# Kernel optimization log

Hardware: AMD Instinct MI355X
Metric: run time of the kernel (lower is better)

## Reference

```python
import jax, jax.numpy as jnp
import numpy as np

B, L, H = 1, 2048, 2048          # batch, seq_len, hidden_size
E, N, K, R = 4096, 16, 4, 128    # intermediate, ssm_state, conv_kernel, dt_rank


def setup_inputs() -> dict:
    key = jax.random.key(0)
    ks = jax.random.split(key, 8)
    s = 0.02
    inp = {
        "hidden_states": jax.random.normal(ks[0], (B, L, H), jnp.float32),
        "in_proj_w": jax.random.normal(ks[1], (2 * E, H), jnp.float32) * s,
        "conv_w": jax.random.normal(ks[2], (E, 1, K), jnp.float32) * s,
        "conv_b": jax.random.normal(ks[3], (E,), jnp.float32) * s,
        "x_proj_w": jax.random.normal(ks[4], (R + 2 * N, E), jnp.float32) * s,
        "dt_proj_w": jax.random.normal(ks[5], (E, R), jnp.float32) * s,
        "dt_proj_b": jax.random.normal(ks[6], (E,), jnp.float32) * s,
        "A_log": jnp.broadcast_to(jnp.log(jnp.arange(1, N + 1, dtype=jnp.float32))[None, :], (E, N)).copy(),
        "D": jnp.ones((E,), jnp.float32),
        "out_proj_w": jax.random.normal(ks[7], (H, E), jnp.float32) * s,
    }
    return inp


def _mamba_mixer(hidden_states, in_proj_w, conv_w, conv_b, x_proj_w,
                 dt_proj_w, dt_proj_b, A_log, D, out_proj_w):
    # in_proj -> [B, L, 2E], split into hidden / gate
    proj = jnp.einsum('blh,eh->ble', hidden_states, in_proj_w)
    h, gate = jnp.split(proj, 2, axis=-1)            # each [B, L, E]

    # depthwise causal conv1d over time, padding K-1 on the left
    h_c = h.transpose(0, 2, 1)                       # [B, E, L]
    h_c = jax.lax.conv_general_dilated(
        h_c, conv_w, window_strides=(1,), padding=[(K - 1, 0)],
        feature_group_count=E, dimension_numbers=('NCH', 'OIH', 'NCH'))
    h_c = h_c + conv_b[None, :, None]
    h = jax.nn.silu(h_c).transpose(0, 2, 1)          # [B, L, E]

    # x_proj -> dt, B, C (input-dependent SSM params)
    ssm = jnp.einsum('ble,pe->blp', h, x_proj_w)     # [B, L, R+2N]
    dt, Bp, Cp = jnp.split(ssm, [R, R + N], axis=-1)
    dt = jax.nn.softplus(jnp.einsum('blr,er->ble', dt, dt_proj_w) + dt_proj_b)  # [B,L,E]

    A = -jnp.exp(A_log)                              # [E, N]
    dA = jnp.exp(dt[..., None] * A)                  # [B, L, E, N]
    dBu = (dt * h)[..., None] * Bp[:, :, None, :]    # [B, L, E, N]

    # selective scan: s_t = dA_t * s_{t-1} + dBu_t
    def step(s, xs):
        dA_t, dBu_t = xs
        s = s * dA_t + dBu_t
        return s, s

    s0 = jnp.zeros((h.shape[0], E, N), h.dtype)
    _, states = jax.lax.scan(step, s0, (dA.transpose(1, 0, 2, 3), dBu.transpose(1, 0, 2, 3)))
    # states: [L, B, E, N]
    y = jnp.einsum('lben,bln->ble', states, Cp)      # [B, L, E]
    y = y + h * D                                    # skip via D
    y = y * jax.nn.silu(gate)                        # gated output
    return jnp.einsum('ble,he->blh', y, out_proj_w)  # [B, L, H]


def reference(hidden_states, in_proj_w, conv_w, conv_b, x_proj_w,
              dt_proj_w, dt_proj_b, A_log, D, out_proj_w):
    return _mamba_mixer(hidden_states, in_proj_w, conv_w, conv_b, x_proj_w,
                        dt_proj_w, dt_proj_b, A_log, D, out_proj_w)
```

## Files before the change

### kernel.cpp

```cpp
#include <hip/hip_runtime.h>

#define LL 2048
#define HH 2048
#define EE 4096
#define NS 16
#define RR 128
#define CT 32
#define NC (LL / CT)
#define BM 128
#define BN 128
#define BK 64

typedef __bf16 bf16x8 __attribute__((ext_vector_type(8)));
typedef float f32x4 __attribute__((ext_vector_type(4)));

__device__ __forceinline__ unsigned short f2bf(float f) {
  union { float f; unsigned int u; } v; v.f = f;
  unsigned int r = v.u + 0x7fffu + ((v.u >> 16) & 1u);
  return (unsigned short)(r >> 16);
}

__device__ __forceinline__ float bf2f(unsigned short u) {
  union { unsigned int i; float f; } v;
  v.i = ((unsigned int)u) << 16;
  return v.f;
}

__device__ __forceinline__ float softplus_fast(float x) {
  if (x > 20.0f) return x;
  float e = __builtin_amdgcn_exp2f(1.44269504f * x);
  return 0.69314718f * __builtin_amdgcn_logf(1.0f + e);
}

__device__ __forceinline__ void async_cp16(const unsigned short* g,
                                           unsigned short* l) {
  __builtin_amdgcn_global_load_lds(
      (const __attribute__((address_space(1))) unsigned int*)g,
      (__attribute__((address_space(3))) unsigned int*)l, 16, 0, 0);
}

#define P_C0 (LL * HH / 4)
#define P_C1 (P_C0 + 2 * EE * HH / 4)
#define P_C2 (P_C1 + 160 * EE / 4)
#define P_C3 (P_C2 + EE * RR / 4)
#define P_C4 (P_C3 + HH * EE / 4)
#define P_C5 (P_C4 + LL * 160 / 4)

__global__ __launch_bounds__(256) void prep_k(
    const float* __restrict__ hs, unsigned short* __restrict__ hsb,
    const float* __restrict__ w1, unsigned short* __restrict__ w1b,
    const float* __restrict__ xw, unsigned short* __restrict__ xwb,
    const float* __restrict__ dtw, unsigned short* __restrict__ dtwb,
    const float* __restrict__ ow, unsigned short* __restrict__ owb,
    float* __restrict__ ssm) {
  int i = blockIdx.x * 256 + threadIdx.x;
  const float* src = nullptr;
  unsigned short* dst = nullptr;
  int k = 0;
  if (i < P_C0)      { src = hs;  dst = hsb;  k = i; }
  else if (i < P_C1) { src = w1;  dst = w1b;  k = i - P_C0; }
  else if (i < P_C2) { src = xw;  dst = xwb;  k = i - P_C1; }
  else if (i < P_C3) { src = dtw; dst = dtwb; k = i - P_C2; }
  else if (i < P_C4) { src = ow;  dst = owb;  k = i - P_C3; }
  else {
    float4 z; z.x = z.y = z.z = z.w = 0.0f;
    reinterpret_cast<float4*>(ssm)[i - P_C4] = z;
    return;
  }
  float4 v = reinterpret_cast<const float4*>(src)[k];
  ushort4 o;
  o.x = f2bf(v.x); o.y = f2bf(v.y); o.z = f2bf(v.z); o.w = f2bf(v.w);
  reinterpret_cast<ushort4*>(dst)[k] = o;
}

template <int EPI>
__global__ __launch_bounds__(512, 2) void gemm256(
    const unsigned short* __restrict__ A,
    const unsigned short* __restrict__ B,
    float* __restrict__ C,
    int M, int N, int K, int tilesM, int splitk,
    float* __restrict__ auxF, unsigned short* __restrict__ auxB) {
  __shared__ __align__(16) unsigned short As[2][16384];
  __shared__ __align__(16) unsigned short Bs[2][16384];

  int bid = blockIdx.x;
  int tnInner = bid & 7;
  int rest = bid >> 3;
  int tm = rest % tilesM;
  int tn = (rest / tilesM) * 8 + tnInner;

  int Kslice = K / splitk;
  int k_begin = blockIdx.y * Kslice;
  int NT = Kslice / 64;

  int tid = threadIdx.x;
  int lane = tid & 63;
  int wave = tid >> 6;
  int wm = wave >> 2;
  int wn = wave & 3;
  int m16 = lane & 15, quad = lane >> 4;

  const unsigned short* Ab = A + (size_t)tm * 256 * K;
  const unsigned short* Bb = B + (size_t)tn * 256 * K;

  int rowS = tid >> 3;
  int gcbS = (tid & 7) ^ (rowS & 7);
  int ldsWB = (tid & ~63) * 8;

  int sw = m16 & 7;
  int coff0 = (quad ^ sw) << 3;
  int coff1 = ((4 + quad) ^ sw) << 3;
  int aoff = (wm * 128 + m16) * 64;
  int boff = (wn * 64 + m16) * 64;

  f32x4 acc[8][4];
#pragma unroll
  for (int i = 0; i < 8; ++i)
#pragma unroll
    for (int j = 0; j < 4; ++j)
#pragma unroll
      for (int t = 0; t < 4; ++t) acc[i][j][t] = 0.0f;

  auto stageA = [&](int bufb, int t, int h) {
    int kt = k_begin + t * 64;
    unsigned short* dst = &As[bufb][0];
#pragma unroll
    for (int c = 2 * h; c < 2 * h + 2; ++c)
      async_cp16(Ab + (size_t)(c * 64 + rowS) * K + kt + gcbS * 8,
                 dst + c * 4096 + ldsWB);
  };
  auto stageB = [&](int bufb, int t, int h) {
    int kt = k_begin + t * 64;
    unsigned short* dst = &Bs[bufb][0];
#pragma unroll
    for (int c = 2 * h; c < 2 * h + 2; ++c)
      async_cp16(Bb + (size_t)(c * 64 + rowS) * K + kt + gcbS * 8,
                 dst + c * 4096 + ldsWB);
  };

  stageA(0, 0, 0); stageA(0, 0, 1);
  stageB(0, 0, 0); stageB(0, 0, 1);
  stageB(1, 1, 0); stageB(1, 1, 1);
  stageA(1, 1, 0);
  asm volatile("s_waitcnt vmcnt(6)" ::: "memory");
  __builtin_amdgcn_s_barrier();

  bf16x8 a[4][2], b0[2][2], b1[2][2];

  for (int t0 = 0; t0 < NT; t0 += 2) {
    int t1 = t0 + 1;
    bool notLast = (t0 + 2 < NT);
    unsigned short* A0 = &As[0][0];
    unsigned short* B0 = &Bs[0][0];
    unsigned short* A1 = &As[1][0];
    unsigned short* B1 = &Bs[1][0];

#pragma unroll
    for (int i = 0; i < 4; ++i) {
      a[i][0] = *reinterpret_cast<const bf16x8*>(&A0[aoff + i * 1024 + coff0]);
      a[i][1] = *reinterpret_cast<const bf16x8*>(&A0[aoff + i * 1024 + coff1]);
    }
#pragma unroll
    for (int j = 0; j < 2; ++j) {
      b0[j][0] = *reinterpret_cast<const bf16x8*>(&B0[boff + j * 1024 + coff0]);
      b0[j][1] = *reinterpret_cast<const bf16x8*>(&B0[boff + j * 1024 + coff1]);
    }
    stageA(1, t1, 1);
    __builtin_amdgcn_s_barrier();
    asm volatile("s_waitcnt lgkmcnt(0)" ::: "memory");
    __builtin_amdgcn_sched_barrier(0);
    __builtin_amdgcn_s_setprio(1);
#pragma unroll
    for (int kk = 0; kk < 2; ++kk)
#pragma unroll
      for (int i = 0; i < 4; ++i)
#pragma unroll
        for (int j = 0; j < 2; ++j)
          acc[i][j] = __builtin_amdgcn_mfma_f32_16x16x32_bf16(
              a[i][kk], b0[j][kk], acc[i][j], 0, 0, 0);
    __builtin_amdgcn_s_setprio(0);
    __builtin_amdgcn_s_barrier();

#pragma unroll
    for (int j = 0; j < 2; ++j) {
      b1[j][0] = *reinterpret_cast<const bf16x8*>(&B0[boff + (2 + j) * 1024 + coff0]);
      b1[j][1] = *reinterpret_cast<const bf16x8*>(&B0[boff + (2 + j) * 1024 + coff1]);
    }
    __builtin_amdgcn_s_barrier();
    asm volatile("s_waitcnt lgkmcnt(0)" ::: "memory");
    __builtin_amdgcn_sched_barrier(0);
    __builtin_amdgcn_s_setprio(1);
#pragma unroll
    for (int kk = 0; kk < 2; ++kk)
#pragma unroll
      for (int i = 0; i < 4; ++i)
#pragma unroll
        for (int j = 0; j < 2; ++j)
          acc[i][2 + j] = __builtin_amdgcn_mfma_f32_16x16x32_bf16(
              a[i][kk], b1[j][kk], acc[i][2 + j], 0, 0, 0);
    __builtin_amdgcn_s_setprio(0);
    __builtin_amdgcn_s_barrier();

#pragma unroll
    for (int i = 0; i < 4; ++i) {
      a[i][0] = *reinterpret_cast<const bf16x8*>(&A0[aoff + (4 + i) * 1024 + coff0]);
      a[i][1] = *reinterpret_cast<const bf16x8*>(&A0[aoff + (4 + i) * 1024 + coff1]);
    }
    if (notLast) stageB(0, t0 + 2, 0);
    __builtin_amdgcn_s_barrier();
    asm volatile("s_waitcnt lgkmcnt(0)" ::: "memory");
    __builtin_amdgcn_sched_barrier(0);
    __builtin_amdgcn_s_setprio(1);
#pragma unroll
    for (int kk = 0; kk < 2; ++kk)
#pragma unroll
      for (int i = 0; i < 4; ++i)
#pragma unroll
        for (int j = 0; j < 2; ++j)
          acc[4 + i][2 + j] = __builtin_amdgcn_mfma_f32_16x16x32_bf16(
              a[i][kk], b1[j][kk], acc[4 + i][2 + j], 0, 0, 0);
    __builtin_amdgcn_s_setprio(0);
    __builtin_amdgcn_s_barrier();

    if (notLast) stageB(0, t0 + 2, 1);
    __builtin_amdgcn_s_setprio(1);
#pragma unroll
    for (int kk = 0; kk < 2; ++kk)
#pragma unroll
      for (int i = 0; i < 4; ++i)
#pragma unroll
        for (int j = 0; j < 2; ++j)
          acc[4 + i][j] = __builtin_amdgcn_mfma_f32_16x16x32_bf16(
              a[i][kk], b0[j][kk], acc[4 + i][j], 0, 0, 0);
    __builtin_amdgcn_s_setprio(0);
    if (notLast) {
      asm volatile("s_waitcnt vmcnt(4)" ::: "memory");
    } else {
      asm volatile("s_waitcnt vmcnt(0)" ::: "memory");
    }
    __builtin_amdgcn_s_barrier();

#pragma unroll
    for (int i = 0; i < 4; ++i) {
      a[i][0] = *reinterpret_cast<const bf16x8*>(&A1[aoff + i * 1024 + coff0]);
      a[i][1] = *reinterpret_cast<const bf16x8*>(&A1[aoff + i * 1024 + coff1]);
    }
#pragma unroll
    for (int j = 0; j < 2; ++j) {
      b0[j][0] = *reinterpret_cast<const bf16x8*>(&B1[boff + j * 1024 + coff0]);
      b0[j][1] = *reinterpret_cast<const bf16x8*>(&B1[boff + j * 1024 + coff1]);
    }
    if (notLast) stageA(0, t0 + 2, 0);
    __builtin_amdgcn_s_barrier();
    asm volatile("s_waitcnt lgkmcnt(0)" ::: "memory");
    __builtin_amdgcn_sched_barrier(0);
    __builtin_amdgcn_s_setprio(1);
#pragma unroll
    for (int kk = 0; kk < 2; ++kk)
#pragma unroll
      for (int i = 0; i < 4; ++i)
#pragma unroll
        for (int j = 0; j < 2; ++j)
          acc[i][j] = __builtin_amdgcn_mfma_f32_16x16x32_bf16(
              a[i][kk], b0[j][kk], acc[i][j], 0, 0, 0);
    __builtin_amdgcn_s_setprio(0);
    __builtin_amdgcn_s_barrier();

#pragma unroll
    for (int j = 0; j < 2; ++j) {
      b1[j][0] = *reinterpret_cast<const bf16x8*>(&B1[boff + (2 + j) * 1024 + coff0]);
      b1[j][1] = *reinterpret_cast<const bf16x8*>(&B1[boff + (2 + j) * 1024 + coff1]);
    }
    if (notLast) stageA(0, t0 + 2, 1);
    __builtin_amdgcn_s_barrier();
    asm volatile("s_waitcnt lgkmcnt(0)" ::: "memory");
    __builtin_amdgcn_sched_barrier(0);
    __builtin_amdgcn_s_setprio(1);
#pragma unroll
    for (int kk = 0; kk < 2; ++kk)
#pragma unroll
      for (int i = 0; i < 4; ++i)
#pragma unroll
        for (int j = 0; j < 2; ++j)
          acc[i][2 + j] = __builtin_amdgcn_mfma_f32_16x16x32_bf16(
              a[i][kk], b1[j][kk], acc[i][2 + j], 0, 0, 0);
    __builtin_amdgcn_s_setprio(0);
    __builtin_amdgcn_s_barrier();

#pragma unroll
    for (int i = 0; i < 4; ++i) {
      a[i][0] = *reinterpret_cast<const bf16x8*>(&A1[aoff + (4 + i) * 1024 + coff0]);
      a[i][1] = *reinterpret_cast<const bf16x8*>(&A1[aoff + (4 + i) * 1024 + coff1]);
    }
    if (notLast) stageB(1, t1 + 2, 0);
    __builtin_amdgcn_s_barrier();
    asm volatile("s_waitcnt lgkmcnt(0)" ::: "memory");
    __builtin_amdgcn_sched_barrier(0);
    __builtin_amdgcn_s_setprio(1);
#pragma unroll
    for (int kk = 0; kk < 2; ++kk)
#pragma unroll
      for (int i = 0; i < 4; ++i)
#pragma unroll
        for (int j = 0; j < 2; ++j)
          acc[4 + i][2 + j] = __builtin_amdgcn_mfma_f32_16x16x32_bf16(
              a[i][kk], b1[j][kk], acc[4 + i][2 + j], 0, 0, 0);
    __builtin_amdgcn_s_setprio(0);
    __builtin_amdgcn_s_barrier();

    if (notLast) { stageB(1, t1 + 2, 1); stageA(1, t1 + 2, 0); }
    __builtin_amdgcn_s_setprio(1);
#pragma unroll
    for (int kk = 0; kk < 2; ++kk)
#pragma unroll
      for (int i = 0; i < 4; ++i)
#pragma unroll
        for (int j = 0; j < 2; ++j)
          acc[4 + i][j] = __builtin_amdgcn_mfma_f32_16x16x32_bf16(
              a[i][kk], b0[j][kk], acc[4 + i][j], 0, 0, 0);
    __builtin_amdgcn_s_setprio(0);
    if (notLast) {
      asm volatile("s_waitcnt vmcnt(6)" ::: "memory");
    }
    __builtin_amdgcn_s_barrier();
  }

  int rowB = tm * 256 + wm * 128;
  int colB = tn * 256 + wn * 64;
  if constexpr (EPI == 1) {
#pragma unroll
    for (int mi = 0; mi < 8; ++mi)
#pragma unroll
      for (int nj = 0; nj < 4; ++nj) {
        int col = colB + nj * 16 + m16;
        int row0 = rowB + mi * 16 + quad * 4;
#pragma unroll
        for (int t4 = 0; t4 < 4; ++t4)
          atomicAdd(&C[(size_t)(row0 + t4) * N + col], acc[mi][nj][t4]);
      }
  } else {
    if (colB < EE) {
#pragma unroll
      for (int mi = 0; mi < 8; ++mi)
#pragma unroll
        for (int nj = 0; nj < 4; ++nj) {
          int col = colB + nj * 16 + m16;
          int row0 = rowB + mi * 16 + quad * 4;
#pragma unroll
          for (int t4 = 0; t4 < 4; ++t4)
            auxF[(size_t)(row0 + t4) * EE + col] = acc[mi][nj][t4];
        }
    } else {
#pragma unroll
      for (int mi = 0; mi < 8; ++mi)
#pragma unroll
        for (int nj = 0; nj < 4; ++nj) {
          int cg = colB + nj * 16 + m16 - EE;
          int row0 = rowB + mi * 16 + quad * 4;
#pragma unroll
          for (int t4 = 0; t4 < 4; ++t4) {
            float v = acc[mi][nj][t4];
            float s = v / (1.0f + __expf(-v));
            auxB[(size_t)(row0 + t4) * EE + cg] = f2bf(s);
          }
        }
    }
  }
}

__global__ __launch_bounds__(256, 2) void gemm128p(
    const unsigned short* __restrict__ A,
    const unsigned short* __restrict__ B,
    float* __restrict__ C,
    int M, int N, int K, int tilesM) {
  __shared__ __align__(16) unsigned short As[2][8192];
  __shared__ __align__(16) unsigned short Bs[2][8192];

  int bid = blockIdx.x;
  int tnInner = bid & 7;
  int rest = bid >> 3;
  int tm = rest % tilesM;
  int tn = (rest / tilesM) * 8 + tnInner;

  int NT = K / 64;

  int tid = threadIdx.x;
  int lane = tid & 63;
  int wave = tid >> 6;
  int wm = wave >> 1;
  int wn = wave & 1;
  int m16 = lane & 15, quad = lane >> 4;

  const unsigned short* Ab = A + (size_t)tm * 128 * K;
  const unsigned short* Bb = B + (size_t)tn * 128 * K;

  int rowS = tid >> 3;
  int gcbS = (tid & 7) ^ (rowS & 7);
  int ldsWB = (tid & ~63) * 8;

  int sw = m16 & 7;
  int coff0 = (quad ^ sw) << 3;
  int coff1 = ((4 + quad) ^ sw) << 3;
  int aoff = (wm * 64 + m16) * 64;
  int boff = (wn * 64 + m16) * 64;

  f32x4 acc[4][4];
#pragma unroll
  for (int i = 0; i < 4; ++i)
#pragma unroll
    for (int j = 0; j < 4; ++j)
#pragma unroll
      for (int t = 0; t < 4; ++t) acc[i][j][t] = 0.0f;

  auto stageA = [&](int bufb, int t, int h) {
    int kt = t * 64;
    unsigned short* dst = &As[bufb][0];
#pragma unroll
    for (int c = 2 * h; c < 2 * h + 2; ++c)
      async_cp16(Ab + (size_t)(c * 32 + rowS) * K + kt + gcbS * 8,
                 dst + c * 2048 + ldsWB);
  };
  auto stageB = [&](int bufb, int t, int h) {
    int kt = t * 64;
    unsigned short* dst = &Bs[bufb][0];
#pragma unroll
    for (int c = 2 * h; c < 2 * h + 2; ++c)
      async_cp16(Bb + (size_t)(c * 32 + rowS) * K + kt + gcbS * 8,
                 dst + c * 2048 + ldsWB);
  };

  stageA(0, 0, 0); stageA(0, 0, 1);
  stageB(0, 0, 0); stageB(0, 0, 1);
  stageB(1, 1, 0); stageB(1, 1, 1);
  stageA(1, 1, 0);
  asm volatile("s_waitcnt vmcnt(6)" ::: "memory");
  __builtin_amdgcn_s_barrier();

  bf16x8 a[2][2], b0[2][2], b1[2][2];

  for (int t0 = 0; t0 < NT; t0 += 2) {
    int t1 = t0 + 1;
    bool notLast = (t0 + 2 < NT);
    unsigned short* A0 = &As[0][0];
    unsigned short* B0 = &Bs[0][0];
    unsigned short* A1 = &As[1][0];
    unsigned short* B1 = &Bs[1][0];

#pragma unroll
    for (int i = 0; i < 2; ++i) {
      a[i][0] = *reinterpret_cast<const bf16x8*>(&A0[aoff + i * 1024 + coff0]);
      a[i][1] = *reinterpret_cast<const bf16x8*>(&A0[aoff + i * 1024 + coff1]);
    }
#pragma unroll
    for (int j = 0; j < 2; ++j) {
      b0[j][0] = *reinterpret_cast<const bf16x8*>(&B0[boff + j * 1024 + coff0]);
      b0[j][1] = *reinterpret_cast<const bf16x8*>(&B0[boff + j * 1024 + coff1]);
    }
    stageA(1, t1, 1);
    __builtin_amdgcn_s_barrier();
    asm volatile("s_waitcnt lgkmcnt(0)" ::: "memory");
    __builtin_amdgcn_sched_barrier(0);
    __builtin_amdgcn_s_setprio(1);
#pragma unroll
    for (int kk = 0; kk < 2; ++kk)
#pragma unroll
      for (int i = 0; i < 2; ++i)
#pragma unroll
        for (int j = 0; j < 2; ++j)
          acc[i][j] = __builtin_amdgcn_mfma_f32_16x16x32_bf16(
              a[i][kk], b0[j][kk], acc[i][j], 0, 0, 0);
    __builtin_amdgcn_s_setprio(0);
    __builtin_amdgcn_s_barrier();

#pragma unroll
    for (int j = 0; j < 2; ++j) {
      b1[j][0] = *reinterpret_cast<const bf16x8*>(&B0[boff + (2 + j) * 1024 + coff0]);
      b1[j][1] = *reinterpret_cast<const bf16x8*>(&B0[boff + (2 + j) * 1024 + coff1]);
    }
    __builtin_amdgcn_s_barrier();
    asm volatile("s_waitcnt lgkmcnt(0)" ::: "memory");
    __builtin_amdgcn_sched_barrier(0);
    __builtin_amdgcn_s_setprio(1);
#pragma unroll
    for (int kk = 0; kk < 2; ++kk)
#pragma unroll
      for (int i = 0; i < 2; ++i)
#pragma unroll
        for (int j = 0; j < 2; ++j)
          acc[i][2 + j] = __builtin_amdgcn_mfma_f32_16x16x32_bf16(
              a[i][kk], b1[j][kk], acc[i][2 + j], 0, 0, 0);
    __builtin_amdgcn_s_setprio(0);
    __builtin_amdgcn_s_barrier();

#pragma unroll
    for (int i = 0; i < 2; ++i) {
      a[i][0] = *reinterpret_cast<const bf16x8*>(&A0[aoff + (2 + i) * 1024 + coff0]);
      a[i][1] = *reinterpret_cast<const bf16x8*>(&A0[aoff + (2 + i) * 1024 + coff1]);
    }
    if (notLast) stageB(0, t0 + 2, 0);
    __builtin_amdgcn_s_barrier();
    asm volatile("s_waitcnt lgkmcnt(0)" ::: "memory");
    __builtin_amdgcn_sched_barrier(0);
    __builtin_amdgcn_s_setprio(1);
#pragma unroll
    for (int kk = 0; kk < 2; ++kk)
#pragma unroll
      for (int i = 0; i < 2; ++i)
#pragma unroll
        for (int j = 0; j < 2; ++j)
          acc[2 + i][2 + j] = __builtin_amdgcn_mfma_f32_16x16x32_bf16(
              a[i][kk], b1[j][kk], acc[2 + i][2 + j], 0, 0, 0);
    __builtin_amdgcn_s_setprio(0);
    __builtin_amdgcn_s_barrier();

    if (notLast) stageB(0, t0 + 2, 1);
    __builtin_amdgcn_s_setprio(1);
#pragma unroll
    for (int kk = 0; kk < 2; ++kk)
#pragma unroll
      for (int i = 0; i < 2; ++i)
#pragma unroll
        for (int j = 0; j < 2; ++j)
          acc[2 + i][j] = __builtin_amdgcn_mfma_f32_16x16x32_bf16(
              a[i][kk], b0[j][kk], acc[2 + i][j], 0, 0, 0);
    __builtin_amdgcn_s_setprio(0);
    if (notLast) {
      asm volatile("s_waitcnt vmcnt(4)" ::: "memory");
    } else {
      asm volatile("s_waitcnt vmcnt(0)" ::: "memory");
    }
    __builtin_amdgcn_s_barrier();

#pragma unroll
    for (int i = 0; i < 2; ++i) {
      a[i][0] = *reinterpret_cast<const bf16x8*>(&A1[aoff + i * 1024 + coff0]);
      a[i][1] = *reinterpret_cast<const bf16x8*>(&A1[aoff + i * 1024 + coff1]);
    }
#pragma unroll
    for (int j = 0; j < 2; ++j) {
      b0[j][0] = *reinterpret_cast<const bf16x8*>(&B1[boff + j * 1024 + coff0]);
      b0[j][1] = *reinterpret_cast<const bf16x8*>(&B1[boff + j * 1024 + coff1]);
    }
    if (notLast) stageA(0, t0 + 2, 0);
    __builtin_amdgcn_s_barrier();
    asm volatile("s_waitcnt lgkmcnt(0)" ::: "memory");
    __builtin_amdgcn_sched_barrier(0);
    __builtin_amdgcn_s_setprio(1);
#pragma unroll
    for (int kk = 0; kk < 2; ++kk)
#pragma unroll
      for (int i = 0; i < 2; ++i)
#pragma unroll
        for (int j = 0; j < 2; ++j)
          acc[i][j] = __builtin_amdgcn_mfma_f32_16x16x32_bf16(
              a[i][kk], b0[j][kk], acc[i][j], 0, 0, 0);
    __builtin_amdgcn_s_setprio(0);
    __builtin_amdgcn_s_barrier();

#pragma unroll
    for (int j = 0; j < 2; ++j) {
      b1[j][0] = *reinterpret_cast<const bf16x8*>(&B1[boff + (2 + j) * 1024 + coff0]);
      b1[j][1] = *reinterpret_cast<const bf16x8*>(&B1[boff + (2 + j) * 1024 + coff1]);
    }
    if (notLast) stageA(0, t0 + 2, 1);
    __builtin_amdgcn_s_barrier();
    asm volatile("s_waitcnt lgkmcnt(0)" ::: "memory");
    __builtin_amdgcn_sched_barrier(0);
    __builtin_amdgcn_s_setprio(1);
#pragma unroll
    for (int kk = 0; kk < 2; ++kk)
#pragma unroll
      for (int i = 0; i < 2; ++i)
#pragma unroll
        for (int j = 0; j < 2; ++j)
          acc[i][2 + j] = __builtin_amdgcn_mfma_f32_16x16x32_bf16(
              a[i][kk], b1[j][kk], acc[i][2 + j], 0, 0, 0);
    __builtin_amdgcn_s_setprio(0);
    __builtin_amdgcn_s_barrier();

#pragma unroll
    for (int i = 0; i < 2; ++i) {
      a[i][0] = *reinterpret_cast<const bf16x8*>(&A1[aoff + (2 + i) * 1024 + coff0]);
      a[i][1] = *reinterpret_cast<const bf16x8*>(&A1[aoff + (2 + i) * 1024 + coff1]);
    }
    if (notLast) stageB(1, t1 + 2, 0);
    __builtin_amdgcn_s_barrier();
    asm volatile("s_waitcnt lgkmcnt(0)" ::: "memory");
    __builtin_amdgcn_sched_barrier(0);
    __builtin_amdgcn_s_setprio(1);
#pragma unroll
    for (int kk = 0; kk < 2; ++kk)
#pragma unroll
      for (int i = 0; i < 2; ++i)
#pragma unroll
        for (int j = 0; j < 2; ++j)
          acc[2 + i][2 + j] = __builtin_amdgcn_mfma_f32_16x16x32_bf16(
              a[i][kk], b1[j][kk], acc[2 + i][2 + j], 0, 0, 0);
    __builtin_amdgcn_s_setprio(0);
    __builtin_amdgcn_s_barrier();

    if (notLast) { stageB(1, t1 + 2, 1); stageA(1, t1 + 2, 0); }
    __builtin_amdgcn_s_setprio(1);
#pragma unroll
    for (int kk = 0; kk < 2; ++kk)
#pragma unroll
      for (int i = 0; i < 2; ++i)
#pragma unroll
        for (int j = 0; j < 2; ++j)
          acc[2 + i][j] = __builtin_amdgcn_mfma_f32_16x16x32_bf16(
              a[i][kk], b0[j][kk], acc[2 + i][j], 0, 0, 0);
    __builtin_amdgcn_s_setprio(0);
    if (notLast) {
      asm volatile("s_waitcnt vmcnt(6)" ::: "memory");
    }
    __builtin_amdgcn_s_barrier();
  }

  int rowB = tm * 128 + wm * 64;
  int colB = tn * 128 + wn * 64;
#pragma unroll
  for (int mi = 0; mi < 4; ++mi)
#pragma unroll
    for (int nj = 0; nj < 4; ++nj) {
      int col = colB + nj * 16 + m16;
      int row0 = rowB + mi * 16 + quad * 4;
#pragma unroll
      for (int t4 = 0; t4 < 4; ++t4)
        C[(size_t)(row0 + t4) * N + col] = acc[mi][nj][t4];
    }
}

template <int EPI>
__global__ __launch_bounds__(256) void gemm_lds_t(
    const unsigned short* __restrict__ A,
    const unsigned short* __restrict__ B,
    float* __restrict__ C,
    int M, int N, int K, int tilesM, int splitk,
    const float* __restrict__ bias, float* __restrict__ auxF,
    unsigned short* __restrict__ auxB) {
  __shared__ __align__(16) unsigned short As[BM * BK];
  __shared__ __align__(16) unsigned short Bs[BN * BK];

  int bid = blockIdx.x;
  int tnInner = bid & 7;
  int rest = bid >> 3;
  int tm = rest % tilesM;
  int tnOuter = rest / tilesM;
  int tn = tnOuter * 8 + tnInner;

  int Kslice = K / splitk;
  int k_begin = blockIdx.y * Kslice;
  int k_end = k_begin + Kslice;

  int tid = threadIdx.x;
  int lane = tid & 63;
  int wave = tid >> 6;
  int wm = wave & 1, wn = wave >> 1;
  int m16 = lane & 15, quad = lane >> 4;

  const unsigned short* Ab = A + (size_t)tm * BM * K;
  const unsigned short* Bb = B + (size_t)tn * BN * K;

  int srow[4], sgcb[4];
#pragma unroll
  for (int it = 0; it < 4; ++it) {
    int blk = it * 256 + tid;
    srow[it] = blk >> 3;
    sgcb[it] = (blk & 7) ^ (srow[it] & 7);
  }
  int ldsbase = (tid & ~63) * 8;

  f32x4 acc[4][4];
#pragma unroll
  for (int i = 0; i < 4; ++i)
#pragma unroll
    for (int j = 0; j < 4; ++j)
#pragma unroll
      for (int t = 0; t < 4; ++t) acc[i][j][t] = 0.0f;

  for (int k0 = k_begin; k0 < k_end; k0 += BK) {
    __syncthreads();
#pragma unroll
    for (int it = 0; it < 4; ++it)
      async_cp16(Ab + (size_t)srow[it] * K + k0 + sgcb[it] * 8,
                 &As[it * 2048 + ldsbase]);
#pragma unroll
    for (int it = 0; it < 4; ++it)
      async_cp16(Bb + (size_t)srow[it] * K + k0 + sgcb[it] * 8,
                 &Bs[it * 2048 + ldsbase]);
    __syncthreads();
#pragma unroll
    for (int kk = 0; kk < 2; ++kk) {
      bf16x8 a[4], b[4];
#pragma unroll
      for (int i = 0; i < 4; ++i) {
        int rr = wm * 64 + i * 16 + m16;
        int cb = (kk << 2) + quad;
        a[i] = *reinterpret_cast<const bf16x8*>(
            &As[rr * BK + ((cb ^ (rr & 7)) << 3)]);
      }
#pragma unroll
      for (int j = 0; j < 4; ++j) {
        int rr = wn * 64 + j * 16 + m16;
        int cb = (kk << 2) + quad;
        b[j] = *reinterpret_cast<const bf16x8*>(
            &Bs[rr * BK + ((cb ^ (rr & 7)) << 3)]);
      }
#pragma unroll
      for (int i = 0; i < 4; ++i)
#pragma unroll
        for (int j = 0; j < 4; ++j)
          acc[i][j] =
              __builtin_amdgcn_mfma_f32_16x16x32_bf16(a[i], b[j], acc[i][j], 0, 0, 0);
    }
  }

  int rowB = tm * BM + wm * 64;
  int colB = tn * BN + wn * 64;
  if constexpr (EPI == 1) {
#pragma unroll
    for (int i = 0; i < 4; ++i)
#pragma unroll
      for (int j = 0; j < 4; ++j) {
        int col = colB + j * 16 + m16;
        int row0 = rowB + i * 16 + quad * 4;
#pragma unroll
        for (int t = 0; t < 4; ++t)
          atomicAdd(&C[(size_t)(row0 + t) * N + col], acc[i][j][t]);
      }
  } else {
#pragma unroll
    for (int i = 0; i < 4; ++i)
#pragma unroll
      for (int j = 0; j < 4; ++j) {
        int col = colB + j * 16 + m16;
        float bv = bias[col];
        int row0 = rowB + i * 16 + quad * 4;
#pragma unroll
        for (int t = 0; t < 4; ++t) {
          float x = acc[i][j][t] + bv;
          auxB[(size_t)(row0 + t) * EE + col] = f2bf(softplus_fast(x));
        }
      }
  }
}

__global__ __launch_bounds__(256) void gemm_bt(
    const unsigned short* __restrict__ A,
    const unsigned short* __restrict__ B,
    float* __restrict__ C,
    int M, int N, int K, int tilesN, int splitk) {
  int bid = blockIdx.x;
  int groupSize = 8 * tilesN;
  int g = bid / groupSize, r = bid % groupSize;
  int tm = g * 8 + (r & 7);
  int tn = r >> 3;

  int Kslice = K / splitk;
  int k_begin = blockIdx.y * Kslice;
  int k_end = k_begin + Kslice;

  int tid = threadIdx.x;
  int wave = tid >> 6, lane = tid & 63;
  int wm = wave & 1, wn = wave >> 1;
  int m16 = lane & 15, quad = lane >> 4;
  int rowBase = tm * 64 + wm * 32;
  int colBase = tn * 128 + wn * 64;

  const unsigned short* a0p = A + (size_t)(rowBase + m16) * K + quad * 8;
  const unsigned short* a1p = A + (size_t)(rowBase + 16 + m16) * K + quad * 8;
  const unsigned short* bp[4];
  bool bok[4];
#pragma unroll
  for (int j = 0; j < 4; ++j) {
    int col = colBase + j * 16 + m16;
    bok[j] = (col < N);
    bp[j] = B + (size_t)(bok[j] ? col : 0) * K + quad * 8;
  }

  f32x4 acc[2][4];
#pragma unroll
  for (int i = 0; i < 2; ++i)
#pragma unroll
    for (int j = 0; j < 4; ++j)
#pragma unroll
      for (int t = 0; t < 4; ++t) acc[i][j][t] = 0.0f;

  bf16x8 zero8;
#pragma unroll
  for (int t = 0; t < 8; ++t) zero8[t] = (__bf16)0.0f;

  for (int k = k_begin; k < k_end; k += 32) {
    bf16x8 a0 = *reinterpret_cast<const bf16x8*>(a0p + k);
    bf16x8 a1 = *reinterpret_cast<const bf16x8*>(a1p + k);
    bf16x8 b[4];
#pragma unroll
    for (int j = 0; j < 4; ++j)
      b[j] = bok[j] ? *reinterpret_cast<const bf16x8*>(bp[j] + k) : zero8;
#pragma unroll
    for (int j = 0; j < 4; ++j) {
      acc[0][j] = __builtin_amdgcn_mfma_f32_16x16x32_bf16(a0, b[j], acc[0][j], 0, 0, 0);
      acc[1][j] = __builtin_amdgcn_mfma_f32_16x16x32_bf16(a1, b[j], acc[1][j], 0, 0, 0);
    }
  }

#pragma unroll
  for (int i = 0; i < 2; ++i)
#pragma unroll
    for (int j = 0; j < 4; ++j) {
      int col = colBase + j * 16 + m16;
      if (col >= N) continue;
      int row0 = rowBase + i * 16 + quad * 4;
      if (splitk == 1) {
#pragma unroll
        for (int t = 0; t < 4; ++t)
          C[(size_t)(row0 + t) * N + col] = acc[i][j][t];
      } else {
#pragma unroll
        for (int t = 0; t < 4; ++t)
          atomicAdd(&C[(size_t)(row0 + t) * N + col], acc[i][j][t]);
      }
    }
}

__global__ __launch_bounds__(256) void conv_silu_k(
    const float* __restrict__ projh, const float* __restrict__ cw,
    const float* __restrict__ cb, unsigned short* __restrict__ hb) {
  int e = blockIdx.x * 256 + threadIdx.x;
  int l0 = blockIdx.y * 16;
  float w0 = cw[e * 4 + 0], w1 = cw[e * 4 + 1];
  float w2 = cw[e * 4 + 2], w3 = cw[e * 4 + 3];
  float bias = cb[e];
  float xm3 = (l0 >= 3) ? projh[(size_t)(l0 - 3) * EE + e] : 0.0f;
  float xm2 = (l0 >= 2) ? projh[(size_t)(l0 - 2) * EE + e] : 0.0f;
  float xm1 = (l0 >= 1) ? projh[(size_t)(l0 - 1) * EE + e] : 0.0f;
#pragma unroll
  for (int t = 0; t < 16; ++t) {
    int l = l0 + t;
    float x0 = projh[(size_t)l * EE + e];
    float acc = bias + w0 * xm3 + w1 * xm2 + w2 * xm1 + w3 * x0;
    float s = acc / (1.0f + __expf(-acc));
    hb[(size_t)l * EE + e] = f2bf(s);
    xm3 = xm2; xm2 = xm1; xm1 = x0;
  }
}

__global__ void dtcast_k(const float* __restrict__ ssm,
                         unsigned short* __restrict__ dtin, int n) {
  int i = blockIdx.x * blockDim.x + threadIdx.x;
  if (i >= n) return;
  int l = i >> 7, r = i & 127;
  dtin[i] = f2bf(ssm[l * 160 + r]);
}

__global__ __launch_bounds__(256) void scan_partA(
    const unsigned short* __restrict__ dtb, const unsigned short* __restrict__ hb,
    const float* __restrict__ ssm, const float* __restrict__ A_log,
    float* __restrict__ P, float* __restrict__ S) {
  int e = blockIdx.y * 256 + threadIdx.x;
  int c = blockIdx.x;
  float Aa[16];
#pragma unroll
  for (int q = 0; q < 4; ++q) {
    float4 a = reinterpret_cast<const float4*>(&A_log[(size_t)e * NS])[q];
    Aa[q * 4 + 0] = -__expf(a.x) * 1.44269504f;
    Aa[q * 4 + 1] = -__expf(a.y) * 1.44269504f;
    Aa[q * 4 + 2] = -__expf(a.z) * 1.44269504f;
    Aa[q * 4 + 3] = -__expf(a.w) * 1.44269504f;
  }
  float s[16], p[16];
#pragma unroll
  for (int n = 0; n < 16; ++n) { s[n] = 0.0f; p[n] = 1.0f; }
  int l0 = c * CT;
#pragma unroll 2
  for (int t = 0; t < CT; ++t) {
    int l = l0 + t;
    size_t o = (size_t)l * EE + e;
    float dtv = bf2f(dtb[o]);
    float hv = bf2f(hb[o]);
    float Bv[16];
#pragma unroll
    for (int q = 0; q < 4; ++q)
      *reinterpret_cast<float4*>(&Bv[q * 4]) =
          reinterpret_cast<const float4*>(&ssm[(size_t)l * 160 + 128])[q];
    float z = dtv * hv;
#pragma unroll
    for (int n = 0; n < 16; ++n) {
      float dA = __builtin_amdgcn_exp2f(dtv * Aa[n]);
      s[n] = s[n] * dA + z * Bv[n];
      p[n] *= dA;
    }
  }
  size_t base = ((size_t)c * EE + e) * NS;
#pragma unroll
  for (int q = 0; q < 4; ++q) {
    reinterpret_cast<float4*>(&P[base])[q] = *reinterpret_cast<float4*>(&p[q * 4]);
    reinterpret_cast<float4*>(&S[base])[q] = *reinterpret_cast<float4*>(&s[q * 4]);
  }
}

__global__ __launch_bounds__(256) void scan_chunkB(
    const float* __restrict__ P, float* __restrict__ S) {
  int gidx = blockIdx.x * 256 + threadIdx.x;
  float s = 0.0f;
  float pv = P[gidx], sv = S[gidx];
  for (int c = 0; c < NC; ++c) {
    float pn = 0.0f, sn = 0.0f;
    if (c + 1 < NC) {
      size_t i2 = (size_t)(c + 1) * (EE * NS) + gidx;
      pn = P[i2];
      sn = S[i2];
    }
    float s_next = s * pv + sv;
    S[(size_t)c * (EE * NS) + gidx] = s;
    s = s_next;
    pv = pn; sv = sn;
  }
}

__global__ __launch_bounds__(256) void scan_partC(
    const unsigned short* __restrict__ dtb, const unsigned short* __restrict__ hb,
    const float* __restrict__ ssm, const float* __restrict__ A_log,
    const float* __restrict__ Dp, const unsigned short* __restrict__ sg,
    const float* __restrict__ Sinit, unsigned short* __restrict__ yb) {
  int e = blockIdx.y * 256 + threadIdx.x;
  int c = blockIdx.x;
  float Aa[16];
#pragma unroll
  for (int q = 0; q < 4; ++q) {
    float4 a = reinterpret_cast<const float4*>(&A_log[(size_t)e * NS])[q];
    Aa[q * 4 + 0] = -__expf(a.x) * 1.44269504f;
    Aa[q * 4 + 1] = -__expf(a.y) * 1.44269504f;
    Aa[q * 4 + 2] = -__expf(a.z) * 1.44269504f;
    Aa[q * 4 + 3] = -__expf(a.w) * 1.44269504f;
  }
  float Dv = Dp[e];
  float s[16];
  size_t base = ((size_t)c * EE + e) * NS;
#pragma unroll
  for (int q = 0; q < 4; ++q)
    *reinterpret_cast<float4*>(&s[q * 4]) =
        reinterpret_cast<const float4*>(&Sinit[base])[q];
  int l0 = c * CT;
#pragma unroll 2
  for (int t = 0; t < CT; ++t) {
    int l = l0 + t;
    size_t o = (size_t)l * EE + e;
    float dtv = bf2f(dtb[o]);
    float hv = bf2f(hb[o]);
    float Bv[16], Cv[16];
#pragma unroll
    for (int q = 0; q < 4; ++q) {
      *reinterpret_cast<float4*>(&Bv[q * 4]) =
          reinterpret_cast<const float4*>(&ssm[(size_t)l * 160 + 128])[q];
      *reinterpret_cast<float4*>(&Cv[q * 4]) =
          reinterpret_cast<const float4*>(&ssm[(size_t)l * 160 + 144])[q];
    }
    float z = dtv * hv;
    float y = 0.0f;
#pragma unroll
    for (int n = 0; n < 16; ++n) {
      float dA = __builtin_amdgcn_exp2f(dtv * Aa[n]);
      s[n] = s[n] * dA + z * Bv[n];
      y += s[n] * Cv[n];
    }
    float gv = bf2f(sg[o]);
    float yv = (y + hv * Dv) * gv;
    yb[o] = f2bf(yv);
  }
}

extern "C" void kernel_launch(void* const* d_in, const int* in_sizes, int n_in,
                              void* d_out, int out_size, void* d_ws, size_t ws_size,
                              hipStream_t stream) {
  const float* hs   = (const float*)d_in[0];
  const float* w1   = (const float*)d_in[1];
  const float* cw   = (const float*)d_in[2];
  const float* cb   = (const float*)d_in[3];
  const float* xw   = (const float*)d_in[4];
  const float* dtw  = (const float*)d_in[5];
  const float* dtb  = (const float*)d_in[6];
  const float* Alog = (const float*)d_in[7];
  const float* Dp   = (const float*)d_in[8];
  const float* ow   = (const float*)d_in[9];
  float* out = (float*)d_out;

  char* ws = (char*)d_ws;
  size_t off = 0;
  auto alloc = [&](size_t b) {
    char* p = ws + off;
    off += (b + 255) & ~(size_t)255;
    return p;
  };
  float* projh = (float*)alloc((size_t)LL * EE * 4);
  unsigned short* sg  = (unsigned short*)alloc((size_t)LL * EE * 2);
  unsigned short* hb  = (unsigned short*)alloc((size_t)LL * EE * 2);
  unsigned short* dtb_buf = (unsigned short*)alloc((size_t)LL * EE * 2);
  unsigned short* w1b = (unsigned short*)alloc((size_t)2 * EE * HH * 2);
  unsigned short* hsb = (unsigned short*)alloc((size_t)LL * HH * 2);
  unsigned short* yb  = (unsigned short*)alloc((size_t)LL * EE * 2);
  unsigned short* owb = (unsigned short*)alloc((size_t)HH * EE * 2);
  unsigned short* xwb = (unsigned short*)alloc((size_t)160 * EE * 2);
  float* ssm = (float*)alloc((size_t)LL * 160 * 4);
  unsigned short* dtin = (unsigned short*)alloc((size_t)LL * RR * 2);
  unsigned short* dtwb = (unsigned short*)alloc((size_t)EE * RR * 2);
  float* Pbuf = (float*)alloc((size_t)NC * EE * NS * 4);
  float* Sbuf = (float*)alloc((size_t)NC * EE * NS * 4);

  prep_k<<<P_C5 / 256, 256, 0, stream>>>(hs, hsb, w1, w1b, xw, xwb, dtw, dtwb,
                                         ow, owb, ssm);

  {
    int tilesM = LL / 256;
    int tilesN = (2 * EE) / 256;
    gemm256<2><<<dim3(tilesM * tilesN, 1), 512, 0, stream>>>(
        hsb, w1b, nullptr, LL, 2 * EE, HH, tilesM, 1, projh, sg);
  }
  conv_silu_k<<<dim3(EE / 256, LL / 16), 256, 0, stream>>>(projh, cw, cb, hb);
  {
    int tilesN = (160 + 127) / 128, tilesM = LL / 64;
    gemm_bt<<<dim3(tilesM * tilesN, 8), 256, 0, stream>>>(
        hb, xwb, ssm, LL, 160, EE, tilesN, 8);
  }
  dtcast_k<<<(LL * RR + 255) / 256, 256, 0, stream>>>(ssm, dtin, LL * RR);
  {
    int tilesN = EE / BN, tilesM = LL / BM;
    gemm_lds_t<4><<<dim3(tilesM * tilesN, 1), 256, 0, stream>>>(
        dtin, dtwb, nullptr, LL, EE, RR, tilesM, 1, dtb, nullptr, dtb_buf);
  }
  scan_partA<<<dim3(NC, EE / 256), 256, 0, stream>>>(dtb_buf, hb, ssm, Alog,
                                                     Pbuf, Sbuf);
  scan_chunkB<<<EE * NS / 256, 256, 0, stream>>>(Pbuf, Sbuf);
  scan_partC<<<dim3(NC, EE / 256), 256, 0, stream>>>(dtb_buf, hb, ssm, Alog, Dp,
                                                     sg, Sbuf, yb);
  {
    int tilesM = LL / 128, tilesN = HH / 128;
    gemm128p<<<dim3(tilesM * tilesN, 1), 256, 0, stream>>>(
        yb, owb, out, LL, HH, EE, tilesM);
  }
}
```

Baseline: 393.0 us.

## Replace split-K atomics with partial buffers plus reduce kernel, reuse gemm_bt for dt_proj

The x_proj split-K GEMM now writes per-slice partials into the output buffer, which is used as scratch, instead of doing atomicAdd into a zeroed ssm buffer. A new reduce kernel sums the partials and emits the bf16 dt input in the same pass, replacing both the zeroing in prep_k and the separate dtcast kernel. The dt_proj GEMM moves from gemm_lds_t to a templated gemm_bt with a fused softplus epilogue. scan_chunkB prefetches two chunks ahead instead of one. This trades atomic contention and one launch for extra partial-buffer traffic, and relies on the output buffer being overwritten later by the final GEMM.

After: 407.2 us. +3.6%, slower.

```diff
diff --git a/kernel.cpp b/kernel.cpp
--- a/kernel.cpp
+++ b/kernel.cpp
@@ -7,9 +7,6 @@
 #define RR 128
 #define CT 32
 #define NC (LL / CT)
-#define BM 128
-#define BN 128
-#define BK 64
 
 typedef __bf16 bf16x8 __attribute__((ext_vector_type(8)));
 typedef float f32x4 __attribute__((ext_vector_type(4)));
@@ -44,29 +41,22 @@
 #define P_C2 (P_C1 + 160 * EE / 4)
 #define P_C3 (P_C2 + EE * RR / 4)
 #define P_C4 (P_C3 + HH * EE / 4)
-#define P_C5 (P_C4 + LL * 160 / 4)
 
 __global__ __launch_bounds__(256) void prep_k(
     const float* __restrict__ hs, unsigned short* __restrict__ hsb,
     const float* __restrict__ w1, unsigned short* __restrict__ w1b,
     const float* __restrict__ xw, unsigned short* __restrict__ xwb,
     const float* __restrict__ dtw, unsigned short* __restrict__ dtwb,
-    const float* __restrict__ ow, unsigned short* __restrict__ owb,
-    float* __restrict__ ssm) {
+    const float* __restrict__ ow, unsigned short* __restrict__ owb) {
   int i = blockIdx.x * 256 + threadIdx.x;
-  const float* src = nullptr;
-  unsigned short* dst = nullptr;
-  int k = 0;
+  const float* src;
+  unsigned short* dst;
+  int k;
   if (i < P_C0)      { src = hs;  dst = hsb;  k = i; }
   else if (i < P_C1) { src = w1;  dst = w1b;  k = i - P_C0; }
   else if (i < P_C2) { src = xw;  dst = xwb;  k = i - P_C1; }
   else if (i < P_C3) { src = dtw; dst = dtwb; k = i - P_C2; }
-  else if (i < P_C4) { src = ow;  dst = owb;  k = i - P_C3; }
-  else {
-    float4 z; z.x = z.y = z.z = z.w = 0.0f;
-    reinterpret_cast<float4*>(ssm)[i - P_C4] = z;
-    return;
-  }
+  else               { src = ow;  dst = owb;  k = i - P_C3; }
   float4 v = reinterpret_cast<const float4*>(src)[k];
   ushort4 o;
   o.x = f2bf(v.x); o.y = f2bf(v.y); o.z = f2bf(v.z); o.w = f2bf(v.w);
@@ -327,18 +317,7 @@
 
   int rowB = tm * 256 + wm * 128;
   int colB = tn * 256 + wn * 64;
-  if constexpr (EPI == 1) {
-#pragma unroll
-    for (int mi = 0; mi < 8; ++mi)
-#pragma unroll
-      for (int nj = 0; nj < 4; ++nj) {
-        int col = colB + nj * 16 + m16;
-        int row0 = rowB + mi * 16 + quad * 4;
-#pragma unroll
-        for (int t4 = 0; t4 < 4; ++t4)
-          atomicAdd(&C[(size_t)(row0 + t4) * N + col], acc[mi][nj][t4]);
-      }
-  } else {
+  if constexpr (EPI == 2) {
     if (colB < EE) {
 #pragma unroll
       for (int mi = 0; mi < 8; ++mi)
@@ -631,125 +610,12 @@
 }
 
 template <int EPI>
-__global__ __launch_bounds__(256) void gemm_lds_t(
-    const unsigned short* __restrict__ A,
-    const unsigned short* __restrict__ B,
-    float* __restrict__ C,
-    int M, int N, int K, int tilesM, int splitk,
-    const float* __restrict__ bias, float* __restrict__ auxF,
-    unsigned short* __restrict__ auxB) {
-  __shared__ __align__(16) unsigned short As[BM * BK];
-  __shared__ __align__(16) unsigned short Bs[BN * BK];
-
-  int bid = blockIdx.x;
-  int tnInner = bid & 7;
-  int rest = bid >> 3;
-  int tm = rest % tilesM;
-  int tnOuter = rest / tilesM;
-  int tn = tnOuter * 8 + tnInner;
-
-  int Kslice = K / splitk;
-  int k_begin = blockIdx.y * Kslice;
-  int k_end = k_begin + Kslice;
-
-  int tid = threadIdx.x;
-  int lane = tid & 63;
-  int wave = tid >> 6;
-  int wm = wave & 1, wn = wave >> 1;
-  int m16 = lane & 15, quad = lane >> 4;
-
-  const unsigned short* Ab = A + (size_t)tm * BM * K;
-  const unsigned short* Bb = B + (size_t)tn * BN * K;
-
-  int srow[4], sgcb[4];
-#pragma unroll
-  for (int it = 0; it < 4; ++it) {
-    int blk = it * 256 + tid;
-    srow[it] = blk >> 3;
-    sgcb[it] = (blk & 7) ^ (srow[it] & 7);
-  }
-  int ldsbase = (tid & ~63) * 8;
-
-  f32x4 acc[4][4];
-#pragma unroll
-  for (int i = 0; i < 4; ++i)
-#pragma unroll
-    for (int j = 0; j < 4; ++j)
-#pragma unroll
-      for (int t = 0; t < 4; ++t) acc[i][j][t] = 0.0f;
-
-  for (int k0 = k_begin; k0 < k_end; k0 += BK) {
-    __syncthreads();
-#pragma unroll
-    for (int it = 0; it < 4; ++it)
-      async_cp16(Ab + (size_t)srow[it] * K + k0 + sgcb[it] * 8,
-                 &As[it * 2048 + ldsbase]);
-#pragma unroll
-    for (int it = 0; it < 4; ++it)
-      async_cp16(Bb + (size_t)srow[it] * K + k0 + sgcb[it] * 8,
-                 &Bs[it * 2048 + ldsbase]);
-    __syncthreads();
-#pragma unroll
-    for (int kk = 0; kk < 2; ++kk) {
-      bf16x8 a[4], b[4];
-#pragma unroll
-      for (int i = 0; i < 4; ++i) {
-        int rr = wm * 64 + i * 16 + m16;
-        int cb = (kk << 2) + quad;
-        a[i] = *reinterpret_cast<const bf16x8*>(
-            &As[rr * BK + ((cb ^ (rr & 7)) << 3)]);
-      }
-#pragma unroll
-      for (int j = 0; j < 4; ++j) {
-        int rr = wn * 64 + j * 16 + m16;
-        int cb = (kk << 2) + quad;
-        b[j] = *reinterpret_cast<const bf16x8*>(
-            &Bs[rr * BK + ((cb ^ (rr & 7)) << 3)]);
-      }
-#pragma unroll
-      for (int i = 0; i < 4; ++i)
-#pragma unroll
-        for (int j = 0; j < 4; ++j)
-          acc[i][j] =
-              __builtin_amdgcn_mfma_f32_16x16x32_bf16(a[i], b[j], acc[i][j], 0, 0, 0);
-    }
-  }
-
-  int rowB = tm * BM + wm * 64;
-  int colB = tn * BN + wn * 64;
-  if constexpr (EPI == 1) {
-#pragma unroll
-    for (int i = 0; i < 4; ++i)
-#pragma unroll
-      for (int j = 0; j < 4; ++j) {
-        int col = colB + j * 16 + m16;
-        int row0 = rowB + i * 16 + quad * 4;
-#pragma unroll
-        for (int t = 0; t < 4; ++t)
-          atomicAdd(&C[(size_t)(row0 + t) * N + col], acc[i][j][t]);
-      }
-  } else {
-#pragma unroll
-    for (int i = 0; i < 4; ++i)
-#pragma unroll
-      for (int j = 0; j < 4; ++j) {
-        int col = colB + j * 16 + m16;
-        float bv = bias[col];
-        int row0 = rowB + i * 16 + quad * 4;
-#pragma unroll
-        for (int t = 0; t < 4; ++t) {
-          float x = acc[i][j][t] + bv;
-          auxB[(size_t)(row0 + t) * EE + col] = f2bf(softplus_fast(x));
-        }
-      }
-  }
-}
-
 __global__ __launch_bounds__(256) void gemm_bt(
     const unsigned short* __restrict__ A,
     const unsigned short* __restrict__ B,
     float* __restrict__ C,
-    int M, int N, int K, int tilesN, int splitk) {
+    int M, int N, int K, int tilesN, int splitk,
+    const float* __restrict__ bias, unsigned short* __restrict__ auxB) {
   int bid = blockIdx.x;
   int groupSize = 8 * tilesN;
   int g = bid / groupSize, r = bid % groupSize;
@@ -804,6 +670,8 @@
     }
   }
 
+  float* Cs = C;
+  if constexpr (EPI == 2) Cs = C + (size_t)blockIdx.y * M * N;
 #pragma unroll
   for (int i = 0; i < 2; ++i)
 #pragma unroll
@@ -811,16 +679,31 @@
       int col = colBase + j * 16 + m16;
       if (col >= N) continue;
       int row0 = rowBase + i * 16 + quad * 4;
-      if (splitk == 1) {
+      if constexpr (EPI == 4) {
+        float bv = bias[col];
 #pragma unroll
         for (int t = 0; t < 4; ++t)
-          C[(size_t)(row0 + t) * N + col] = acc[i][j][t];
+          auxB[(size_t)(row0 + t) * N + col] =
+              f2bf(softplus_fast(acc[i][j][t] + bv));
       } else {
 #pragma unroll
         for (int t = 0; t < 4; ++t)
-          atomicAdd(&C[(size_t)(row0 + t) * N + col], acc[i][j][t]);
+          Cs[(size_t)(row0 + t) * N + col] = acc[i][j][t];
       }
     }
+}
+
+__global__ __launch_bounds__(256) void xreduce_k(
+    const float* __restrict__ xp, float* __restrict__ ssm,
+    unsigned short* __restrict__ dtin) {
+  int i = blockIdx.x * 256 + threadIdx.x;
+  float s = 0.0f;
+#pragma unroll
+  for (int k = 0; k < 8; ++k)
+    s += xp[(size_t)k * (LL * 160) + i];
+  ssm[i] = s;
+  int l = i / 160, r = i - l * 160;
+  if (r < 128) dtin[l * 128 + r] = f2bf(s);
 }
 
 __global__ __launch_bounds__(256) void conv_silu_k(
@@ -845,14 +728,6 @@
   }
 }
 
-__global__ void dtcast_k(const float* __restrict__ ssm,
-                         unsigned short* __restrict__ dtin, int n) {
-  int i = blockIdx.x * blockDim.x + threadIdx.x;
-  if (i >= n) return;
-  int l = i >> 7, r = i & 127;
-  dtin[i] = f2bf(ssm[l * 160 + r]);
-}
-
 __global__ __launch_bounds__(256) void scan_partA(
     const unsigned short* __restrict__ dtb, const unsigned short* __restrict__ hb,
     const float* __restrict__ ssm, const float* __restrict__ A_log,
@@ -902,19 +777,21 @@
 __global__ __launch_bounds__(256) void scan_chunkB(
     const float* __restrict__ P, float* __restrict__ S) {
   int gidx = blockIdx.x * 256 + threadIdx.x;
+  const size_t stride = (size_t)EE * NS;
   float s = 0.0f;
-  float pv = P[gidx], sv = S[gidx];
+  float pv0 = P[gidx], sv0 = S[gidx];
+  float pv1 = P[stride + gidx], sv1 = S[stride + gidx];
   for (int c = 0; c < NC; ++c) {
     float pn = 0.0f, sn = 0.0f;
-    if (c + 1 < NC) {
-      size_t i2 = (size_t)(c + 1) * (EE * NS) + gidx;
+    if (c + 2 < NC) {
+      size_t i2 = (size_t)(c + 2) * stride + gidx;
       pn = P[i2];
       sn = S[i2];
     }
-    float s_next = s * pv + sv;
-    S[(size_t)c * (EE * NS) + gidx] = s;
+    float s_next = s * pv0 + sv0;
+    S[(size_t)c * stride + gidx] = s;
     s = s_next;
-    pv = pn; sv = sn;
+    pv0 = pv1; sv0 = sv1; pv1 = pn; sv1 = sn;
   }
 }
 
@@ -1006,9 +883,10 @@
   unsigned short* dtwb = (unsigned short*)alloc((size_t)EE * RR * 2);
   float* Pbuf = (float*)alloc((size_t)NC * EE * NS * 4);
   float* Sbuf = (float*)alloc((size_t)NC * EE * NS * 4);
-
-  prep_k<<<P_C5 / 256, 256, 0, stream>>>(hs, hsb, w1, w1b, xw, xwb, dtw, dtwb,
-                                         ow, owb, ssm);
+  float* xpart = out;
+
+  prep_k<<<P_C4 / 256, 256, 0, stream>>>(hs, hsb, w1, w1b, xw, xwb, dtw, dtwb,
+                                         ow, owb);
 
   {
     int tilesM = LL / 256;
@@ -1019,14 +897,14 @@
   conv_silu_k<<<dim3(EE / 256, LL / 16), 256, 0, stream>>>(projh, cw, cb, hb);
   {
     int tilesN = (160 + 127) / 128, tilesM = LL / 64;
-    gemm_bt<<<dim3(tilesM * tilesN, 8), 256, 0, stream>>>(
-        hb, xwb, ssm, LL, 160, EE, tilesN, 8);
-  }
-  dtcast_k<<<(LL * RR + 255) / 256, 256, 0, stream>>>(ssm, dtin, LL * RR);
+    gemm_bt<2><<<dim3(tilesM * tilesN, 8), 256, 0, stream>>>(
+        hb, xwb, xpart, LL, 160, EE, tilesN, 8, nullptr, nullptr);
+  }
+  xreduce_k<<<LL * 160 / 256, 256, 0, stream>>>(xpart, ssm, dtin);
   {
-    int tilesN = EE / BN, tilesM = LL / BM;
-    gemm_lds_t<4><<<dim3(tilesM * tilesN, 1), 256, 0, stream>>>(
-        dtin, dtwb, nullptr, LL, EE, RR, tilesM, 1, dtb, nullptr, dtb_buf);
+    int tilesN = EE / 128, tilesM = LL / 64;
+    gemm_bt<4><<<dim3(tilesM * tilesN, 1), 256, 0, stream>>>(
+        dtin, dtwb, nullptr, LL, EE, RR, tilesN, 1, dtb, dtb_buf);
   }
   scan_partA<<<dim3(NC, EE / 256), 256, 0, stream>>>(dtb_buf, hb, ssm, Alog,
                                                      Pbuf, Sbuf);
```
